# Optimization experiments

Hardware: AMD Instinct MI355X
Metric: run time of the kernel (lower is better)

The kernel has to match this reference:

```python
import jax, jax.numpy as jnp
import numpy as np

N_HEAD, D_HEAD, D_MODEL = 16, 64, 1024
QLEN, MLEN, BSZ = 512, 512, 8
KLEN = QLEN + MLEN
SCALE = 1.0 / D_HEAD ** 0.5
LN_EPS = 1e-5


def rel_shift(x):
    # x: [qlen, klen, bsz, n_head] -- Transformer-XL pad/reshape shift trick
    q, k, b, n = x.shape
    x_pad = jnp.pad(x, ((0, 0), (1, 0), (0, 0), (0, 0)))
    x_pad = x_pad.reshape(k + 1, q, b, n)
    return x_pad[1:].reshape(q, k, b, n)


def setup_inputs() -> dict:
    key = jax.random.key(0)
    ks = jax.random.split(key, 10)
    s = 0.02
    return {
        'w': jax.random.normal(ks[0], (QLEN, BSZ, D_MODEL), jnp.float32),
        'r': jax.random.normal(ks[1], (KLEN, D_MODEL), jnp.float32),
        'mems': jax.random.normal(ks[2], (MLEN, BSZ, D_MODEL), jnp.float32),
        'r_w_bias': jax.random.normal(ks[3], (N_HEAD, D_HEAD), jnp.float32) * s,
        'r_r_bias': jax.random.normal(ks[4], (N_HEAD, D_HEAD), jnp.float32) * s,
        'Wq': jax.random.normal(ks[5], (N_HEAD * D_HEAD, D_MODEL), jnp.float32) * s,
        'Wkv': jax.random.normal(ks[6], (2 * N_HEAD * D_HEAD, D_MODEL), jnp.float32) * s,
        'Wr': jax.random.normal(ks[7], (N_HEAD * D_HEAD, D_MODEL), jnp.float32) * s,
        'br': jnp.zeros((N_HEAD * D_HEAD,), jnp.float32),
        'Wo': jax.random.normal(ks[8], (D_MODEL, N_HEAD * D_HEAD), jnp.float32) * s,
        'bo': jnp.zeros((D_MODEL,), jnp.float32),
        'gamma': jnp.ones((D_MODEL,), jnp.float32),
        'beta': jnp.zeros((D_MODEL,), jnp.float32),
    }


def reference(w, r, mems, r_w_bias, r_r_bias, Wq, Wkv, Wr, br, Wo, bo, gamma, beta):
    qlen, bsz, _ = w.shape
    cat = jnp.concatenate([mems, w], axis=0)           # [klen, b, d]
    klen = cat.shape[0]
    mlen = klen - qlen

    q = (w @ Wq.T).reshape(qlen, bsz, N_HEAD, D_HEAD)   # [i, b, n, d]
    kv = (cat @ Wkv.T).reshape(klen, bsz, N_HEAD, 2 * D_HEAD)
    k, v = kv[..., :D_HEAD], kv[..., D_HEAD:]           # [j, b, n, d]
    rk = (r @ Wr.T + br).reshape(klen, N_HEAD, D_HEAD)  # [j, n, d]

    AC = jnp.einsum('ibnd,jbnd->ijbn', q + r_w_bias, k)
    BD = jnp.einsum('ibnd,jnd->ijbn', q + r_r_bias, rk)
    BD = rel_shift(BD)
    score = (AC + BD) * SCALE                           # [i, j, b, n]

    # causal mask with memory: query i attends to keys j <= i + mlen
    i_idx = jnp.arange(qlen)[:, None]
    j_idx = jnp.arange(klen)[None, :]
    mask = j_idx > (i_idx + mlen)
    score = jnp.where(mask[:, :, None, None], -1e30, score)

    prob = jax.nn.softmax(score, axis=1)
    attn_vec = jnp.einsum('ijbn,jbnd->ibnd', prob, v).reshape(qlen, bsz, N_HEAD * D_HEAD)
    attn_out = attn_vec @ Wo.T + bo

    # IdentityResidualGate: x + relu(y), then LayerNorm
    y = w + jax.nn.relu(attn_out)
    mu = jnp.mean(y, axis=-1, keepdims=True)
    var = jnp.mean(jnp.square(y - mu), axis=-1, keepdims=True)
    return (y - mu) * jax.lax.rsqrt(var + LN_EPS) * gamma + beta
```

## Files before the change

kernel.cpp:

```cpp
#include <hip/hip_runtime.h>
#include <hip/hip_bf16.h>
#include <cstdint>
#include <cstddef>

typedef __attribute__((ext_vector_type(4))) float f32x4;
typedef __attribute__((ext_vector_type(8))) short bf16x8;
using u16 = unsigned short;

#define ATT_SCALE 0.125f

__device__ __forceinline__ u16 f2b(float f) {
    union { float f; uint32_t u; } x; x.f = f;
    uint32_t r = x.u + 0x7fffu + ((x.u >> 16) & 1u);
    return (u16)(r >> 16);
}

#define GLDS16(g, s)                                                        \
    __builtin_amdgcn_global_load_lds(                                       \
        (const __attribute__((address_space(1))) uint32_t*)(g),             \
        (__attribute__((address_space(3))) uint32_t*)(s), 16, 0, 0)

__global__ __launch_bounds__(256) void prep_kernel(
    const float* __restrict__ mems, const float* __restrict__ w,
    const float* __restrict__ r, const float* __restrict__ Wq,
    const float* __restrict__ Wkv, const float* __restrict__ Wr,
    const float* __restrict__ Wo, u16* __restrict__ cat_b,
    u16* __restrict__ r_b, u16* __restrict__ Wq_b, u16* __restrict__ Wkv_b,
    u16* __restrict__ Wr_b, u16* __restrict__ Wo_b) {
    int bid = blockIdx.x;
    if (bid < 8192) {
        int col4 = threadIdx.x;
        float4 v;
        int b, oj;
        if (bid < 4096) {
            v = reinterpret_cast<const float4*>(mems)[(size_t)bid * 256 + col4];
            b = bid & 7; oj = bid >> 3;
        } else {
            int rrow = bid - 4096;
            v = reinterpret_cast<const float4*>(w)[(size_t)rrow * 256 + col4];
            b = rrow & 7; oj = 512 + (rrow >> 3);
        }
        uint2 o;
        o.x = (uint32_t)f2b(v.x) | ((uint32_t)f2b(v.y) << 16);
        o.y = (uint32_t)f2b(v.z) | ((uint32_t)f2b(v.w) << 16);
        reinterpret_cast<uint2*>(cat_b)[(size_t)(b * 1024 + oj) * 256 + col4] = o;
        return;
    }
    bid -= 8192;
    const float4* src;
    uint2* dst;
    if (bid < 1024)      { src = (const float4*)r;   dst = (uint2*)r_b; }
    else if (bid < 2048) { src = (const float4*)Wq;  dst = (uint2*)Wq_b;  bid -= 1024; }
    else if (bid < 4096) { src = (const float4*)Wkv; dst = (uint2*)Wkv_b; bid -= 2048; }
    else if (bid < 5120) { src = (const float4*)Wr;  dst = (uint2*)Wr_b;  bid -= 4096; }
    else                 { src = (const float4*)Wo;  dst = (uint2*)Wo_b;  bid -= 5120; }
    int idx = bid * 256 + threadIdx.x;
    float4 v = src[idx];
    uint2 o;
    o.x = (uint32_t)f2b(v.x) | ((uint32_t)f2b(v.y) << 16);
    o.y = (uint32_t)f2b(v.z) | ((uint32_t)f2b(v.w) << 16);
    dst[idx] = o;
}

__global__ __launch_bounds__(256) void gemm_all(
    const u16* __restrict__ catb, const u16* __restrict__ Wkvb,
    const u16* __restrict__ Wqb, const u16* __restrict__ rb,
    const u16* __restrict__ Wrb, const float* __restrict__ bw,
    const float* __restrict__ brr, const float* __restrict__ br,
    u16* __restrict__ qwb, u16* __restrict__ qrb, u16* __restrict__ kb,
    u16* __restrict__ vtb, u16* __restrict__ rkb) {
    __shared__ uint4 sA[128][8];
    __shared__ uint4 sB[128][8];
    const int idx = (blockIdx.x & 7) * 168 + (blockIdx.x >> 3);
    const u16 *A, *B;
    int N, bx, by, epi;
    if (idx < 1024) {
        epi = 1; B = Wkvb; N = 2048; bx = idx & 63; by = idx >> 6;
        A = catb + (size_t)bx * 128 * 1024;
    } else if (idx < 1280) {
        epi = 0; B = Wqb; N = 1024;
        int l = idx - 1024; bx = l & 31; by = l >> 5;
        int bm0 = bx * 128;
        A = catb + ((size_t)(bm0 >> 9) * 1024 + 512 + (bm0 & 511)) * 1024;
    } else {
        epi = 2; B = Wrb; N = 1024;
        int l = idx - 1280; bx = l & 7; by = l >> 3;
        A = rb + (size_t)bx * 128 * 1024;
    }
    const int tid = threadIdx.x;
    const int wid = tid >> 6, lane = tid & 63;
    const int lr = lane & 15, lg = lane >> 4;
    const int bm = bx * 128, bn = by * 128;
    const int wm = (wid >> 1) * 64, wn = (wid & 1) * 64;
    const int srow = tid >> 3, scol = tid & 7;
    f32x4 acc[4][4] = {};

    for (int k0 = 0; k0 < 1024; k0 += 64) {
#pragma unroll
        for (int p = 0; p < 4; p++) {
            int row = p * 32 + srow;
            GLDS16(A + (size_t)row * 1024 + k0 + scol * 8, &sA[row][scol]);
            GLDS16(B + (size_t)(bn + row) * 1024 + k0 + scol * 8, &sB[row][scol]);
        }
        __syncthreads();
#pragma unroll
        for (int ks = 0; ks < 2; ks++) {
            bf16x8 af[4], bfr[4];
#pragma unroll
            for (int x = 0; x < 4; x++) {
                af[x] = *reinterpret_cast<const bf16x8*>(&sA[wm + x * 16 + lr][ks * 4 + lg]);
                bfr[x] = *reinterpret_cast<const bf16x8*>(&sB[wn + x * 16 + lr][ks * 4 + lg]);
            }
#pragma unroll
            for (int mi = 0; mi < 4; mi++)
#pragma unroll
                for (int ni = 0; ni < 4; ni++)
                    acc[mi][ni] = __builtin_amdgcn_mfma_f32_16x16x32_bf16(
                        af[mi], bfr[ni], acc[mi][ni], 0, 0, 0);
        }
        __syncthreads();
    }
#pragma unroll
    for (int mi = 0; mi < 4; mi++)
#pragma unroll
        for (int ni = 0; ni < 4; ni++) {
            const int m0 = bm + wm + mi * 16 + lg * 4;
            const int c = bn + wn + ni * 16 + lr;
            if (epi == 1) {
                const int b = m0 >> 10, j0 = m0 & 1023;
                const int n = c >> 7, dd = c & 127;
                if (dd < 64) {
#pragma unroll
                    for (int rr = 0; rr < 4; rr++)
                        kb[(((size_t)(b * 16 + n)) * 1024 + j0 + rr) * 64 + dd] =
                            f2b(acc[mi][ni][rr]);
                } else {
                    uint2 pk;
                    pk.x = (uint32_t)f2b(acc[mi][ni][0]) | ((uint32_t)f2b(acc[mi][ni][1]) << 16);
                    pk.y = (uint32_t)f2b(acc[mi][ni][2]) | ((uint32_t)f2b(acc[mi][ni][3]) << 16);
                    *reinterpret_cast<uint2*>(
                        vtb + (((size_t)(b * 16 + n)) * 64 + (dd - 64)) * 1024 + j0) = pk;
                }
            } else if (epi == 0) {
#pragma unroll
                for (int rr = 0; rr < 4; rr++) {
                    int m = m0 + rr;
                    qwb[(size_t)m * 1024 + c] = f2b(acc[mi][ni][rr] + bw[c]);
                    qrb[(size_t)m * 1024 + c] = f2b(acc[mi][ni][rr] + brr[c]);
                }
            } else {
                const int nh = c >> 6, d = c & 63;
#pragma unroll
                for (int rr = 0; rr < 4; rr++)
                    rkb[((size_t)nh * 1024 + m0 + rr) * 64 + d] = f2b(acc[mi][ni][rr] + br[c]);
            }
        }
}

__global__ __launch_bounds__(256) void gemm_out(const u16* __restrict__ A,
                                                const u16* __restrict__ B,
                                                const float* __restrict__ wres,
                                                const float* __restrict__ bo,
                                                float* __restrict__ y) {
    __shared__ uint4 sA[128][8];
    __shared__ uint4 sB[128][8];
    const int tid = threadIdx.x;
    const int wid = tid >> 6, lane = tid & 63;
    const int lr = lane & 15, lg = lane >> 4;
    const int bm = blockIdx.x * 128, bn = blockIdx.y * 128;
    const int wm = (wid >> 1) * 64, wn = (wid & 1) * 64;
    const int srow = tid >> 3, scol = tid & 7;
    f32x4 acc[4][4] = {};

    for (int k0 = 0; k0 < 1024; k0 += 64) {
#pragma unroll
        for (int p = 0; p < 4; p++) {
            int row = p * 32 + srow;
            GLDS16(A + (size_t)(bm + row) * 1024 + k0 + scol * 8, &sA[row][scol]);
            GLDS16(B + (size_t)(bn + row) * 1024 + k0 + scol * 8, &sB[row][scol]);
        }
        __syncthreads();
#pragma unroll
        for (int ks = 0; ks < 2; ks++) {
            bf16x8 af[4], bfr[4];
#pragma unroll
            for (int x = 0; x < 4; x++) {
                af[x] = *reinterpret_cast<const bf16x8*>(&sA[wm + x * 16 + lr][ks * 4 + lg]);
                bfr[x] = *reinterpret_cast<const bf16x8*>(&sB[wn + x * 16 + lr][ks * 4 + lg]);
            }
#pragma unroll
            for (int mi = 0; mi < 4; mi++)
#pragma unroll
                for (int ni = 0; ni < 4; ni++)
                    acc[mi][ni] = __builtin_amdgcn_mfma_f32_16x16x32_bf16(
                        af[mi], bfr[ni], acc[mi][ni], 0, 0, 0);
        }
        __syncthreads();
    }
#pragma unroll
    for (int mi = 0; mi < 4; mi++)
#pragma unroll
        for (int ni = 0; ni < 4; ni++)
#pragma unroll
            for (int rr = 0; rr < 4; rr++) {
                int m = bm + wm + mi * 16 + lg * 4 + rr;
                int c = bn + wn + ni * 16 + lr;
                y[(size_t)m * 1024 + c] =
                    wres[(size_t)m * 1024 + c] + fmaxf(acc[mi][ni][rr] + bo[c], 0.0f);
            }
}

__global__ __launch_bounds__(256, 2) void attn_kernel(const u16* __restrict__ qw,
                                                      const u16* __restrict__ qr,
                                                      const u16* __restrict__ kbuf,
                                                      const u16* __restrict__ vt,
                                                      const u16* __restrict__ rkb,
                                                      u16* __restrict__ attnv) {
    __shared__ uint4 ksh[64][8];
    __shared__ uint4 vsh[64][8];
    __shared__ uint4 rsh[128][8];
    __shared__ float bds[4][16][82];
    __shared__ u16 ps[4][16][72];
    const int bid = blockIdx.x;
    const int wg = (bid & 7) * 128 + (bid >> 3);
    const int i0 = (wg & 7) * 64;
    const int bnid = wg >> 3;
    const int b = bnid & 7, n = bnid >> 3;
    const int tid = threadIdx.x, wid = tid >> 6, lane = tid & 63;
    const int lr = lane & 15, lg = lane >> 4;
    const int it = i0 + wid * 16;

    const u16* qwp = qw + ((size_t)(b * 512 + it + lr)) * 1024 + n * 64;
    const u16* qrp = qr + ((size_t)(b * 512 + it + lr)) * 1024 + n * 64;
    bf16x8 aqw[2], aqr[2];
#pragma unroll
    for (int ks = 0; ks < 2; ks++) {
        aqw[ks] = *reinterpret_cast<const bf16x8*>(qwp + (ks * 4 + lg) * 8);
        aqr[ks] = *reinterpret_cast<const bf16x8*>(qrp + (ks * 4 + lg) * 8);
    }
    const u16* kp = kbuf + ((size_t)(b * 16 + n)) * 65536;
    const u16* vp = vt + ((size_t)(b * 16 + n)) * 65536;
    const u16* rp = rkb + (size_t)n * 65536;

    f32x4 acc[4] = {};
    float lpart[4] = {0.f, 0.f, 0.f, 0.f};
    const int xs = lr & 7;
    const int rbase = 48 - 16 * wid;

    const int nt = (i0 + 639) >> 6;
    for (int t = 0; t < nt; t++) {
        const int j0 = t << 6;
        const int jrb = j0 + 448 - i0;
#pragma unroll
        for (int inst = 0; inst < 2; inst++) {
            int gi = wid * 128 + inst * 64 + lane;
            int row = gi >> 3, c = gi & 7;
            int cs = (c ^ (row & 7)) * 8;
            GLDS16(kp + (size_t)(j0 + row) * 64 + cs,
                   (char*)ksh + (size_t)(wid * 128 + inst * 64) * 16);
            GLDS16(vp + (size_t)row * 1024 + j0 + cs,
                   (char*)vsh + (size_t)(wid * 128 + inst * 64) * 16);
        }
#pragma unroll
        for (int inst = 0; inst < 4; inst++) {
            int gi = wid * 256 + inst * 64 + lane;
            int row = gi >> 3, c = gi & 7;
            int grow = jrb + row;
            if (grow > 1023) grow = 1023;
            GLDS16(rp + (size_t)grow * 64 + (c ^ (row & 7)) * 8,
                   (char*)rsh + (size_t)(wid * 256 + inst * 64) * 16);
        }
        __syncthreads();

        f32x4 s[4] = {};
#pragma unroll
        for (int fj = 0; fj < 4; fj++)
#pragma unroll
            for (int ks = 0; ks < 2; ks++) {
                bf16x8 bk = *reinterpret_cast<const bf16x8*>(
                    &ksh[fj * 16 + lr][(ks * 4 + lg) ^ xs]);
                s[fj] = __builtin_amdgcn_mfma_f32_16x16x32_bf16(aqw[ks], bk, s[fj], 0, 0, 0);
            }
        f32x4 bd[5] = {};
#pragma unroll
        for (int fb = 0; fb < 5; fb++) {
            int rel = rbase + fb * 16 + lr;
#pragma unroll
            for (int ks = 0; ks < 2; ks++) {
                bf16x8 brk = *reinterpret_cast<const bf16x8*>(
                    &rsh[rel][(ks * 4 + lg) ^ xs]);
                bd[fb] = __builtin_amdgcn_mfma_f32_16x16x32_bf16(aqr[ks], brk, bd[fb], 0, 0, 0);
            }
        }
#pragma unroll
        for (int fb = 0; fb < 5; fb++)
#pragma unroll
            for (int rr = 0; rr < 4; rr++)
                bds[wid][lg * 4 + rr][fb * 16 + lr] = bd[fb][rr];

#pragma unroll
        for (int fj = 0; fj < 4; fj++)
#pragma unroll
            for (int rr = 0; rr < 4; rr++) {
                const int di = lg * 4 + rr;
                float v = (s[fj][rr] + bds[wid][di][fj * 16 + lr + 15 - di]) * ATT_SCALE;
                float e = (j0 + fj * 16 + lr <= it + di + 512) ? __expf(v) : 0.0f;
                lpart[rr] += e;
                ps[wid][di][fj * 16 + lr] = f2b(e);
            }
#pragma unroll
        for (int kc = 0; kc < 2; kc++) {
            bf16x8 ap = *reinterpret_cast<const bf16x8*>(&ps[wid][lr][kc * 32 + lg * 8]);
#pragma unroll
            for (int nd = 0; nd < 4; nd++) {
                bf16x8 bv = *reinterpret_cast<const bf16x8*>(
                    &vsh[nd * 16 + lr][(kc * 4 + lg) ^ xs]);
                acc[nd] = __builtin_amdgcn_mfma_f32_16x16x32_bf16(ap, bv, acc[nd], 0, 0, 0);
            }
        }
        __syncthreads();
    }
    float l[4];
#pragma unroll
    for (int rr = 0; rr < 4; rr++) {
        float x = lpart[rr];
        x += __shfl_xor(x, 1);
        x += __shfl_xor(x, 2);
        x += __shfl_xor(x, 4);
        x += __shfl_xor(x, 8);
        l[rr] = x;
    }
#pragma unroll
    for (int nd = 0; nd < 4; nd++)
#pragma unroll
        for (int rr = 0; rr < 4; rr++) {
            int i = it + lg * 4 + rr;
            int d = nd * 16 + lr;
            attnv[((size_t)i * 8 + b) * 1024 + n * 64 + d] = f2b(acc[nd][rr] / l[rr]);
        }
}

__global__ __launch_bounds__(256) void ln_kernel(const float* __restrict__ y,
                                                 const float* __restrict__ gamma,
                                                 const float* __restrict__ beta,
                                                 float* __restrict__ out) {
    __shared__ float rs[8];
    int row = blockIdx.x, tid = threadIdx.x;
    const float4 v = reinterpret_cast<const float4*>(y + (size_t)row * 1024)[tid];
    float s = v.x + v.y + v.z + v.w;
    float s2 = v.x * v.x + v.y * v.y + v.z * v.z + v.w * v.w;
#pragma unroll
    for (int m = 1; m < 64; m <<= 1) {
        s += __shfl_xor(s, m);
        s2 += __shfl_xor(s2, m);
    }
    if ((tid & 63) == 0) {
        rs[tid >> 6] = s;
        rs[4 + (tid >> 6)] = s2;
    }
    __syncthreads();
    s = rs[0] + rs[1] + rs[2] + rs[3];
    s2 = rs[4] + rs[5] + rs[6] + rs[7];
    float mu = s * (1.0f / 1024.0f);
    float var = s2 * (1.0f / 1024.0f) - mu * mu;
    float inv = rsqrtf(var + 1e-5f);
    float4 g = reinterpret_cast<const float4*>(gamma)[tid];
    float4 be = reinterpret_cast<const float4*>(beta)[tid];
    float4 o;
    o.x = (v.x - mu) * inv * g.x + be.x;
    o.y = (v.y - mu) * inv * g.y + be.y;
    o.z = (v.z - mu) * inv * g.z + be.z;
    o.w = (v.w - mu) * inv * g.w + be.w;
    reinterpret_cast<float4*>(out + (size_t)row * 1024)[tid] = o;
}

extern "C" void kernel_launch(void* const* d_in, const int* in_sizes, int n_in,
                              void* d_out, int out_size, void* d_ws, size_t ws_size,
                              hipStream_t stream) {
    (void)in_sizes; (void)n_in; (void)out_size; (void)ws_size;
    const float* w_in  = (const float*)d_in[0];
    const float* r_in  = (const float*)d_in[1];
    const float* mems  = (const float*)d_in[2];
    const float* bw    = (const float*)d_in[3];
    const float* brr   = (const float*)d_in[4];
    const float* Wq    = (const float*)d_in[5];
    const float* Wkv   = (const float*)d_in[6];
    const float* Wr    = (const float*)d_in[7];
    const float* br    = (const float*)d_in[8];
    const float* Wo    = (const float*)d_in[9];
    const float* bo    = (const float*)d_in[10];
    const float* gamma = (const float*)d_in[11];
    const float* beta  = (const float*)d_in[12];

    char* base = (char*)d_ws;
    size_t off = 0;
    auto alloc = [&](size_t bytes) -> char* {
        char* p = base + off;
        off += (bytes + 255) & ~(size_t)255;
        return p;
    };
    u16* cat_b = (u16*)alloc((size_t)8192 * 1024 * 2);
    u16* r_b   = (u16*)alloc((size_t)1024 * 1024 * 2);
    u16* Wq_b  = (u16*)alloc((size_t)1024 * 1024 * 2);
    u16* Wkv_b = (u16*)alloc((size_t)2048 * 1024 * 2);
    u16* Wr_b  = (u16*)alloc((size_t)1024 * 1024 * 2);
    u16* Wo_b  = (u16*)alloc((size_t)1024 * 1024 * 2);
    u16* qw_b  = (u16*)alloc((size_t)4096 * 1024 * 2);
    u16* qr_b  = (u16*)alloc((size_t)4096 * 1024 * 2);
    u16* k_b   = (u16*)alloc((size_t)128 * 1024 * 64 * 2);
    u16* vt_b  = (u16*)alloc((size_t)128 * 64 * 1024 * 2);
    u16* rk_b  = (u16*)alloc((size_t)16 * 1024 * 64 * 2);
    u16* av_b  = (u16*)alloc((size_t)4096 * 1024 * 2);
    float* y = (float*)cat_b;

    prep_kernel<<<14336, 256, 0, stream>>>(mems, w_in, r_in, Wq, Wkv, Wr, Wo,
                                           cat_b, r_b, Wq_b, Wkv_b, Wr_b, Wo_b);

    gemm_all<<<1344, 256, 0, stream>>>(cat_b, Wkv_b, Wq_b, r_b, Wr_b,
                                       bw, brr, br,
                                       qw_b, qr_b, k_b, vt_b, rk_b);

    attn_kernel<<<1024, 256, 0, stream>>>(qw_b, qr_b, k_b, vt_b, rk_b, av_b);

    gemm_out<<<dim3(32, 8), 256, 0, stream>>>(av_b, Wo_b, w_in, bo, y);

    ln_kernel<<<4096, 256, 0, stream>>>(y, gamma, beta, (float*)d_out);
}
```

Measured before the change: 221.9 us.

## Double-buffer K/V tiles in attention and load rel-pos keys directly to registers

The attention kernel now double-buffers the K and V shared-memory tiles, prefetching the next tile while the current one is computed. The rel-position key tile is no longer staged through shared memory; each wave loads its own rk fragments straight from global memory into registers. The gemm block-index swizzle is also removed in favour of linear ordering. The aim is to hide global load latency and cut shared-memory use. The costs are redundant global reads of rk across waves and a possible L2 locality loss in the GEMM. The loop still syncs only once per iteration, so prefetching into the other buffer while it may still be read looks racy.

```diff
diff --git a/kernel.cpp b/kernel.cpp
--- a/kernel.cpp
+++ b/kernel.cpp
@@ -71,7 +71,7 @@
     u16* __restrict__ vtb, u16* __restrict__ rkb) {
     __shared__ uint4 sA[128][8];
     __shared__ uint4 sB[128][8];
-    const int idx = (blockIdx.x & 7) * 168 + (blockIdx.x >> 3);
+    const int idx = blockIdx.x;
     const u16 *A, *B;
     int N, bx, by, epi;
     if (idx < 1024) {
@@ -216,9 +216,8 @@
                                                       const u16* __restrict__ vt,
                                                       const u16* __restrict__ rkb,
                                                       u16* __restrict__ attnv) {
-    __shared__ uint4 ksh[64][8];
-    __shared__ uint4 vsh[64][8];
-    __shared__ uint4 rsh[128][8];
+    __shared__ uint4 ksh[2][64][8];
+    __shared__ uint4 vsh[2][64][8];
     __shared__ float bds[4][16][82];
     __shared__ u16 ps[4][16][72];
     const int bid = blockIdx.x;
@@ -246,52 +245,65 @@
     float lpart[4] = {0.f, 0.f, 0.f, 0.f};
     const int xs = lr & 7;
     const int rbase = 48 - 16 * wid;
-
     const int nt = (i0 + 639) >> 6;
+
+#pragma unroll
+    for (int inst = 0; inst < 2; inst++) {
+        int gi = wid * 128 + inst * 64 + lane;
+        int row = gi >> 3, c = gi & 7;
+        int cs = (c ^ (row & 7)) * 8;
+        GLDS16(kp + (size_t)row * 64 + cs,
+               (char*)ksh + (size_t)(wid * 128 + inst * 64) * 16);
+        GLDS16(vp + (size_t)row * 1024 + cs,
+               (char*)vsh + (size_t)(wid * 128 + inst * 64) * 16);
+    }
+    __syncthreads();
+
     for (int t = 0; t < nt; t++) {
         const int j0 = t << 6;
         const int jrb = j0 + 448 - i0;
-#pragma unroll
-        for (int inst = 0; inst < 2; inst++) {
-            int gi = wid * 128 + inst * 64 + lane;
-            int row = gi >> 3, c = gi & 7;
-            int cs = (c ^ (row & 7)) * 8;
-            GLDS16(kp + (size_t)(j0 + row) * 64 + cs,
-                   (char*)ksh + (size_t)(wid * 128 + inst * 64) * 16);
-            GLDS16(vp + (size_t)row * 1024 + j0 + cs,
-                   (char*)vsh + (size_t)(wid * 128 + inst * 64) * 16);
-        }
-#pragma unroll
-        for (int inst = 0; inst < 4; inst++) {
-            int gi = wid * 256 + inst * 64 + lane;
-            int row = gi >> 3, c = gi & 7;
-            int grow = jrb + row;
-            if (grow > 1023) grow = 1023;
-            GLDS16(rp + (size_t)grow * 64 + (c ^ (row & 7)) * 8,
-                   (char*)rsh + (size_t)(wid * 256 + inst * 64) * 16);
-        }
-        __syncthreads();
-
+        const int cur = t & 1;
+        if (t + 1 < nt) {
+            const int j0n = j0 + 64;
+#pragma unroll
+            for (int inst = 0; inst < 2; inst++) {
+                int gi = wid * 128 + inst * 64 + lane;
+                int row = gi >> 3, c = gi & 7;
+                int cs = (c ^ (row & 7)) * 8;
+                GLDS16(kp + (size_t)(j0n + row) * 64 + cs,
+                       (char*)ksh + (size_t)(cur ^ 1) * 8192 +
+                           (size_t)(wid * 128 + inst * 64) * 16);
+                GLDS16(vp + (size_t)row * 1024 + j0n + cs,
+                       (char*)vsh + (size_t)(cur ^ 1) * 8192 +
+                           (size_t)(wid * 128 + inst * 64) * 16);
+            }
+        }
+        bf16x8 rkr[5][2];
+#pragma unroll
+        for (int fb = 0; fb < 5; fb++) {
+            int row = jrb + rbase + fb * 16 + lr;
+            if (row > 1023) row = 1023;
+#pragma unroll
+            for (int ks = 0; ks < 2; ks++)
+                rkr[fb][ks] = *reinterpret_cast<const bf16x8*>(
+                    rp + (size_t)row * 64 + (ks * 4 + lg) * 8);
+        }
         f32x4 s[4] = {};
 #pragma unroll
         for (int fj = 0; fj < 4; fj++)
 #pragma unroll
             for (int ks = 0; ks < 2; ks++) {
                 bf16x8 bk = *reinterpret_cast<const bf16x8*>(
-                    &ksh[fj * 16 + lr][(ks * 4 + lg) ^ xs]);
+                    &ksh[cur][fj * 16 + lr][(ks * 4 + lg) ^ xs]);
                 s[fj] = __builtin_amdgcn_mfma_f32_16x16x32_bf16(aqw[ks], bk, s[fj], 0, 0, 0);
             }
         f32x4 bd[5] = {};
 #pragma unroll
-        for (int fb = 0; fb < 5; fb++) {
-            int rel = rbase + fb * 16 + lr;
-#pragma unroll
-            for (int ks = 0; ks < 2; ks++) {
-                bf16x8 brk = *reinterpret_cast<const bf16x8*>(
-                    &rsh[rel][(ks * 4 + lg) ^ xs]);
-                bd[fb] = __builtin_amdgcn_mfma_f32_16x16x32_bf16(aqr[ks], brk, bd[fb], 0, 0, 0);
-            }
-        }
+        for (int fb = 0; fb < 5; fb++)
+#pragma unroll
+            for (int ks = 0; ks < 2; ks++)
+                bd[fb] = __builtin_amdgcn_mfma_f32_16x16x32_bf16(aqr[ks], rkr[fb][ks],
+                                                                 bd[fb], 0, 0, 0);
 #pragma unroll
         for (int fb = 0; fb < 5; fb++)
 #pragma unroll
@@ -314,7 +326,7 @@
 #pragma unroll
             for (int nd = 0; nd < 4; nd++) {
                 bf16x8 bv = *reinterpret_cast<const bf16x8*>(
-                    &vsh[nd * 16 + lr][(kc * 4 + lg) ^ xs]);
+                    &vsh[cur][nd * 16 + lr][(kc * 4 + lg) ^ xs]);
                 acc[nd] = __builtin_amdgcn_mfma_f32_16x16x32_bf16(ap, bv, acc[nd], 0, 0, 0);
             }
         }
```

Result: slower. 239.8 us (+8.0%).

## Split KV projection into 256x256 double-buffered swizzled GEMM kernel

Applied to the files above, without the earlier changes.

Moves the large KV projection out of the fused gemm_all launch into a dedicated kernel with 256x256 tiles, 512 threads, LDS double buffering and an XOR swizzle to avoid bank conflicts. Q and R projections stay in a separate 128x128 kernel. The larger tiles raise arithmetic intensity and the prefetch overlaps global loads with MFMA work. In exchange there is an extra launch, only 256 blocks for the KV GEMM (roughly one wave on 256 CUs), and higher register pressure from the 8x4 accumulator array.

```diff
diff --git a/kernel.cpp b/kernel.cpp
--- a/kernel.cpp
+++ b/kernel.cpp
@@ -62,29 +62,106 @@
     dst[idx] = o;
 }
 
-__global__ __launch_bounds__(256) void gemm_all(
-    const u16* __restrict__ catb, const u16* __restrict__ Wkvb,
-    const u16* __restrict__ Wqb, const u16* __restrict__ rb,
-    const u16* __restrict__ Wrb, const float* __restrict__ bw,
-    const float* __restrict__ brr, const float* __restrict__ br,
-    u16* __restrict__ qwb, u16* __restrict__ qrb, u16* __restrict__ kb,
-    u16* __restrict__ vtb, u16* __restrict__ rkb) {
+__global__ __launch_bounds__(512, 1) void kv_gemm(const u16* __restrict__ catb,
+                                                  const u16* __restrict__ Wkvb,
+                                                  u16* __restrict__ kb,
+                                                  u16* __restrict__ vtb) {
+    __shared__ u16 sA[2][256][64];
+    __shared__ u16 sB[2][256][64];
+    const int tid = threadIdx.x;
+    const int wid = tid >> 6, lane = tid & 63;
+    const int lr = lane & 15, lg = lane >> 4;
+    const int bm = blockIdx.x * 256, bn = blockIdx.y * 256;
+    const int Wm = (wid >> 2) * 128, Wn = (wid & 3) * 64;
+    const int srow = tid >> 3, scol = tid & 7;
+    const int xs = lr & 7;
+    const u16* A = catb + (size_t)bm * 1024;
+    const u16* B = Wkvb + (size_t)bn * 1024;
+    f32x4 acc[8][4] = {};
+
+#pragma unroll
+    for (int p = 0; p < 4; p++) {
+        int row = p * 64 + srow;
+        int cs = (scol ^ (row & 7)) * 8;
+        GLDS16(A + (size_t)row * 1024 + cs, &sA[0][row][scol * 8]);
+        GLDS16(B + (size_t)row * 1024 + cs, &sB[0][row][scol * 8]);
+    }
+    __syncthreads();
+
+    int cur = 0;
+    for (int t = 0; t < 16; t++) {
+        if (t < 15) {
+            const int k0n = (t + 1) * 64;
+#pragma unroll
+            for (int p = 0; p < 4; p++) {
+                int row = p * 64 + srow;
+                int cs = (scol ^ (row & 7)) * 8;
+                GLDS16(A + (size_t)row * 1024 + k0n + cs, &sA[cur ^ 1][row][scol * 8]);
+                GLDS16(B + (size_t)row * 1024 + k0n + cs, &sB[cur ^ 1][row][scol * 8]);
+            }
+        }
+#pragma unroll
+        for (int ks = 0; ks < 2; ks++) {
+            bf16x8 af[8], bfr[4];
+#pragma unroll
+            for (int mi = 0; mi < 8; mi++)
+                af[mi] = *reinterpret_cast<const bf16x8*>(
+                    &sA[cur][Wm + mi * 16 + lr][((ks * 4 + lg) ^ xs) * 8]);
+#pragma unroll
+            for (int ni = 0; ni < 4; ni++)
+                bfr[ni] = *reinterpret_cast<const bf16x8*>(
+                    &sB[cur][Wn + ni * 16 + lr][((ks * 4 + lg) ^ xs) * 8]);
+#pragma unroll
+            for (int mi = 0; mi < 8; mi++)
+#pragma unroll
+                for (int ni = 0; ni < 4; ni++)
+                    acc[mi][ni] = __builtin_amdgcn_mfma_f32_16x16x32_bf16(
+                        af[mi], bfr[ni], acc[mi][ni], 0, 0, 0);
+        }
+        __syncthreads();
+        cur ^= 1;
+    }
+#pragma unroll
+    for (int mi = 0; mi < 8; mi++)
+#pragma unroll
+        for (int ni = 0; ni < 4; ni++) {
+            const int m0 = bm + Wm + mi * 16 + lg * 4;
+            const int c = bn + Wn + ni * 16 + lr;
+            const int b = m0 >> 10, j0 = m0 & 1023;
+            const int n = c >> 7, dd = c & 127;
+            if (dd < 64) {
+#pragma unroll
+                for (int rr = 0; rr < 4; rr++)
+                    kb[(((size_t)(b * 16 + n)) * 1024 + j0 + rr) * 64 + dd] =
+                        f2b(acc[mi][ni][rr]);
+            } else {
+                uint2 pk;
+                pk.x = (uint32_t)f2b(acc[mi][ni][0]) | ((uint32_t)f2b(acc[mi][ni][1]) << 16);
+                pk.y = (uint32_t)f2b(acc[mi][ni][2]) | ((uint32_t)f2b(acc[mi][ni][3]) << 16);
+                *reinterpret_cast<uint2*>(
+                    vtb + (((size_t)(b * 16 + n)) * 64 + (dd - 64)) * 1024 + j0) = pk;
+            }
+        }
+}
+
+__global__ __launch_bounds__(256) void qr_gemm(
+    const u16* __restrict__ catb, const u16* __restrict__ Wqb,
+    const u16* __restrict__ rb, const u16* __restrict__ Wrb,
+    const float* __restrict__ bw, const float* __restrict__ brr,
+    const float* __restrict__ br, u16* __restrict__ qwb,
+    u16* __restrict__ qrb, u16* __restrict__ rkb) {
     __shared__ uint4 sA[128][8];
     __shared__ uint4 sB[128][8];
-    const int idx = (blockIdx.x & 7) * 168 + (blockIdx.x >> 3);
+    const int idx = blockIdx.x;
     const u16 *A, *B;
-    int N, bx, by, epi;
-    if (idx < 1024) {
-        epi = 1; B = Wkvb; N = 2048; bx = idx & 63; by = idx >> 6;
-        A = catb + (size_t)bx * 128 * 1024;
-    } else if (idx < 1280) {
-        epi = 0; B = Wqb; N = 1024;
-        int l = idx - 1024; bx = l & 31; by = l >> 5;
+    int bx, by, epi;
+    if (idx < 256) {
+        epi = 0; B = Wqb; bx = idx & 31; by = idx >> 5;
         int bm0 = bx * 128;
         A = catb + ((size_t)(bm0 >> 9) * 1024 + 512 + (bm0 & 511)) * 1024;
     } else {
-        epi = 2; B = Wrb; N = 1024;
-        int l = idx - 1280; bx = l & 7; by = l >> 3;
+        epi = 2; B = Wrb;
+        int l = idx - 256; bx = l & 7; by = l >> 3;
         A = rb + (size_t)bx * 128 * 1024;
     }
     const int tid = threadIdx.x;
@@ -126,22 +203,7 @@
         for (int ni = 0; ni < 4; ni++) {
             const int m0 = bm + wm + mi * 16 + lg * 4;
             const int c = bn + wn + ni * 16 + lr;
-            if (epi == 1) {
-                const int b = m0 >> 10, j0 = m0 & 1023;
-                const int n = c >> 7, dd = c & 127;
-                if (dd < 64) {
-#pragma unroll
-                    for (int rr = 0; rr < 4; rr++)
-                        kb[(((size_t)(b * 16 + n)) * 1024 + j0 + rr) * 64 + dd] =
-                            f2b(acc[mi][ni][rr]);
-                } else {
-                    uint2 pk;
-                    pk.x = (uint32_t)f2b(acc[mi][ni][0]) | ((uint32_t)f2b(acc[mi][ni][1]) << 16);
-                    pk.y = (uint32_t)f2b(acc[mi][ni][2]) | ((uint32_t)f2b(acc[mi][ni][3]) << 16);
-                    *reinterpret_cast<uint2*>(
-                        vtb + (((size_t)(b * 16 + n)) * 64 + (dd - 64)) * 1024 + j0) = pk;
-                }
-            } else if (epi == 0) {
+            if (epi == 0) {
 #pragma unroll
                 for (int rr = 0; rr < 4; rr++) {
                     int m = m0 + rr;
@@ -416,9 +478,9 @@
     prep_kernel<<<14336, 256, 0, stream>>>(mems, w_in, r_in, Wq, Wkv, Wr, Wo,
                                            cat_b, r_b, Wq_b, Wkv_b, Wr_b, Wo_b);
 
-    gemm_all<<<1344, 256, 0, stream>>>(cat_b, Wkv_b, Wq_b, r_b, Wr_b,
-                                       bw, brr, br,
-                                       qw_b, qr_b, k_b, vt_b, rk_b);
+    kv_gemm<<<dim3(32, 8), 512, 0, stream>>>(cat_b, Wkv_b, k_b, vt_b);
+    qr_gemm<<<320, 256, 0, stream>>>(cat_b, Wq_b, r_b, Wr_b, bw, brr, br,
+                                     qw_b, qr_b, rk_b);
 
     attn_kernel<<<1024, 256, 0, stream>>>(qw_b, qr_b, k_b, vt_b, rk_b, av_b);
 
```

Measured after the change: 202.1 us. -8.9%, faster.
